# Kernel tuning notes

Measured on AMD Instinct MI355X. Metric: run time of the kernel, lower is better.

## Reference

```python
import jax, jax.numpy as jnp
import numpy as np

NUM_HEADS = 8
NUM_LEVELS = 4
NUM_POINTS = 4
EMBED_DIM = 256
HEAD_DIM = EMBED_DIM // NUM_HEADS  # 32
SUM_POINTS = NUM_LEVELS * NUM_POINTS  # 16
OFFSET_SCALE = 0.5
SPATIAL = [(80, 80), (40, 40), (20, 20), (10, 10)]


def _bilinear_gather(v_flat, x, y, H, W):
    """grid_sample(bilinear, padding zeros, align_corners=False) via gathers.
    v_flat: (BN, c, H*W); x, y: (BN, Lq, P) pixel coords. -> (BN, c, Lq*P)"""
    BN = v_flat.shape[0]
    x0 = jnp.floor(x)
    y0 = jnp.floor(y)
    wx1 = x - x0
    wy1 = y - y0

    def corner(xi, yi, w):
        valid = (xi >= 0) & (xi <= W - 1) & (yi >= 0) & (yi <= H - 1)
        xc = jnp.clip(xi, 0, W - 1).astype(jnp.int32)
        yc = jnp.clip(yi, 0, H - 1).astype(jnp.int32)
        idx = (yc * W + xc).reshape(BN, -1)  # (BN, Lq*P)
        g = jnp.take_along_axis(v_flat, idx[:, None, :], axis=2)  # (BN, c, Lq*P)
        return g * (w * valid).reshape(BN, 1, -1)

    return (corner(x0, y0, (1.0 - wx1) * (1.0 - wy1))
            + corner(x0 + 1.0, y0, wx1 * (1.0 - wy1))
            + corner(x0, y0 + 1.0, (1.0 - wx1) * wy1)
            + corner(x0 + 1.0, y0 + 1.0, wx1 * wy1))


def setup_inputs() -> dict:
    key = jax.random.key(0)
    ks = jax.random.split(key, 6)
    bs, Lq = 16, 300
    spatial = np.array(SPATIAL, dtype=np.int64)
    Lv = int((spatial[:, 0] * spatial[:, 1]).sum())  # 8500

    query = jax.random.normal(ks[0], (bs, Lq, EMBED_DIM), jnp.float32)
    reference_points = jax.random.uniform(ks[1], (bs, Lq, 1, 4), jnp.float32)  # cx,cy,w,h in (0,1)
    value = jax.random.normal(ks[2], (bs, NUM_HEADS, HEAD_DIM, Lv), jnp.float32)

    W_off = jax.random.normal(ks[3], (EMBED_DIM, NUM_HEADS * SUM_POINTS * 2), jnp.float32) * 0.01
    # bias from _reset_parameters grid init
    thetas = np.arange(NUM_HEADS, dtype=np.float32) * (2.0 * np.pi / NUM_HEADS)
    grid = np.stack([np.cos(thetas), np.sin(thetas)], -1)
    grid = grid / np.abs(grid).max(-1, keepdims=True)
    grid = np.tile(grid.reshape(NUM_HEADS, 1, 2), (1, SUM_POINTS, 1))
    scaling = np.concatenate([np.arange(1, NUM_POINTS + 1) for _ in range(NUM_LEVELS)]).reshape(1, -1, 1)
    b_off = jnp.asarray((grid * scaling).reshape(-1), jnp.float32)

    W_attn = jax.random.normal(ks[4], (EMBED_DIM, NUM_HEADS * SUM_POINTS), jnp.float32) * 0.01
    b_attn = jnp.zeros((NUM_HEADS * SUM_POINTS,), jnp.float32)
    num_points_scale = jnp.full((SUM_POINTS,), 1.0 / NUM_POINTS, jnp.float32)

    return {"query": query, "reference_points": reference_points, "value": value,
            "value_spatial_shapes": spatial, "W_off": W_off, "b_off": b_off,
            "W_attn": W_attn, "b_attn": b_attn, "num_points_scale": num_points_scale}


def reference(query, reference_points, value, value_spatial_shapes,
              W_off, b_off, W_attn, b_attn, num_points_scale):
    bs, Lq, _ = query.shape
    BN = bs * NUM_HEADS

    off = (query @ W_off + b_off).reshape(bs, Lq, NUM_HEADS, SUM_POINTS, 2)
    attn = jax.nn.softmax((query @ W_attn + b_attn).reshape(bs, Lq, NUM_HEADS, SUM_POINTS), axis=-1)

    # box branch: reference_points (bs, Lq, 1, 4); [..., 2:] = wh scales offsets
    offset = off * num_points_scale[:, None] * reference_points[:, :, None, :, 2:] * OFFSET_SCALE
    loc = reference_points[:, :, None, :, :2] + offset  # (bs, Lq, H, SUM_POINTS, 2) in [0,1]

    grids = 2.0 * loc - 1.0
    grids = jnp.transpose(grids, (0, 2, 1, 3, 4)).reshape(BN, Lq, SUM_POINTS, 2)
    attn = jnp.transpose(attn, (0, 2, 1, 3)).reshape(BN, 1, Lq, SUM_POINTS)

    shapes = np.asarray(value_spatial_shapes)
    lvl_sizes = (shapes[:, 0] * shapes[:, 1]).tolist()
    v_levels = jnp.split(value.reshape(BN, HEAD_DIM, -1), np.cumsum(lvl_sizes)[:-1], axis=2)
    g_levels = jnp.split(grids, np.arange(NUM_POINTS, SUM_POINTS, NUM_POINTS), axis=2)

    sampled = []
    for (H, W), v_l, g_l in zip(shapes.tolist(), v_levels, g_levels):
        # align_corners=False pixel coords
        x = (g_l[..., 0] + 1.0) * (W * 0.5) - 0.5
        y = (g_l[..., 1] + 1.0) * (H * 0.5) - 0.5
        s = _bilinear_gather(v_l, x, y, H, W).reshape(BN, HEAD_DIM, Lq, NUM_POINTS)
        sampled.append(s)
    sampled = jnp.concatenate(sampled, axis=-1)  # (BN, c, Lq, SUM_POINTS)

    out = (sampled * attn).sum(-1)  # (BN, c, Lq)
    out = out.reshape(bs, NUM_HEADS * HEAD_DIM, Lq).transpose(0, 2, 1)  # (bs, Lq, embed_dim)
    return out
```

## Files before the change

kernel.cpp:

```cpp
#include <hip/hip_runtime.h>
#include <hip/hip_bf16.h>
#include <math.h>

#define BS 16
#define LQ 300
#define NH 8
#define HD 32
#define SP 16
#define ED 256
#define LV 8500
#define NB_BLK 300
#define NTR_BLK (133 * 128)

static __device__ __forceinline__ int imin(int a, int b) { return a < b ? a : b; }
static __device__ __forceinline__ int imax(int a, int b) { return a > b ? a : b; }

static __device__ __forceinline__ unsigned short f2bf(float x) {
    unsigned u = __float_as_uint(x);
    unsigned r = (u + 0x7fffu + ((u >> 16) & 1u)) >> 16;
    return (unsigned short)r;
}

__global__ __launch_bounds__(256) void kF(const float* __restrict__ query,
                                          const float* __restrict__ refp,
                                          const float* __restrict__ Woff,
                                          const float* __restrict__ boff,
                                          const float* __restrict__ Wattn,
                                          const float* __restrict__ battn,
                                          const float* __restrict__ nps,
                                          float* __restrict__ la,
                                          const float* __restrict__ v,
                                          __hip_bfloat16* __restrict__ vt,
                                          int nb) {
    __shared__ float s[16 * 384];
    __shared__ float red[2][16][8][4];
    const int tid = threadIdx.x;

    if ((int)blockIdx.x >= nb) {
        const int t   = blockIdx.x - nb;
        const int bn  = t / 133;
        const int lv0 = (t - bn * 133) * 64;
        float* tile = s;
        {
            const int c  = tid >> 3;
            const int l4 = (tid & 7) * 4;
            const float* src = v + (size_t)bn * (HD * LV) + (size_t)c * LV + lv0;
#pragma unroll
            for (int i = 0; i < 2; ++i) {
                int off = l4 + i * 32;
                if (lv0 + off < LV) {
                    float4 x = *reinterpret_cast<const float4*>(src + off);
                    float* tp = tile + c * 66 + off;
                    *reinterpret_cast<float2*>(tp)     = make_float2(x.x, x.y);
                    *reinterpret_cast<float2*>(tp + 2) = make_float2(x.z, x.w);
                }
            }
        }
        __syncthreads();
        {
            const int lv = tid >> 2;
            const int c8 = (tid & 3) * 8;
            if (lv0 + lv < LV) {
                unsigned pk[4];
#pragma unroll
                for (int j = 0; j < 4; ++j) {
                    float f0 = tile[(c8 + 2 * j) * 66 + lv];
                    float f1 = tile[(c8 + 2 * j + 1) * 66 + lv];
                    pk[j] = (unsigned)f2bf(f0) | ((unsigned)f2bf(f1) << 16);
                }
                uint4 o = make_uint4(pk[0], pk[1], pk[2], pk[3]);
                *reinterpret_cast<uint4*>((char*)vt +
                    ((size_t)bn * LV + lv0 + lv) * (HD * 2) + c8 * 2) = o;
            }
        }
        return;
    }

    float* qbuf = s;
    float* lbuf = s;
    const int gq0 = blockIdx.x * 16;

    const float* qsrc = query + (size_t)gq0 * ED;
#pragma unroll
    for (int i = 0; i < 16; ++i) qbuf[tid + 256 * i] = qsrc[tid + 256 * i];
    __syncthreads();

    const int qi = tid >> 5;
    const int cl = tid & 31;
    const float* qa = qbuf + qi * ED;
    const float* qb = qbuf + (qi + 8) * ED;

    float a0[4] = {0,0,0,0}, a1[4] = {0,0,0,0}, a2[4] = {0,0,0,0};
    float c0[4] = {0,0,0,0}, c1[4] = {0,0,0,0}, c2[4] = {0,0,0,0};
    const float4* w0 = (const float4*)(Woff + cl * 4);
    const float4* w1 = (const float4*)(Woff + 128 + cl * 4);
    const float4* w2 = (const float4*)(Wattn + cl * 4);
#pragma unroll 4
    for (int k = 0; k < ED; ++k) {
        float va = qa[k], vb = qb[k];
        float4 x0 = w0[k * 64];
        float4 x1 = w1[k * 64];
        float4 x2 = w2[k * 32];
        a0[0] += va * x0.x; a0[1] += va * x0.y; a0[2] += va * x0.z; a0[3] += va * x0.w;
        a1[0] += va * x1.x; a1[1] += va * x1.y; a1[2] += va * x1.z; a1[3] += va * x1.w;
        a2[0] += va * x2.x; a2[1] += va * x2.y; a2[2] += va * x2.z; a2[3] += va * x2.w;
        c0[0] += vb * x0.x; c0[1] += vb * x0.y; c0[2] += vb * x0.z; c0[3] += vb * x0.w;
        c1[0] += vb * x1.x; c1[1] += vb * x1.y; c1[2] += vb * x1.z; c1[3] += vb * x1.w;
        c2[0] += vb * x2.x; c2[1] += vb * x2.y; c2[2] += vb * x2.z; c2[3] += vb * x2.w;
    }
    __syncthreads();
    {
        float* ra = lbuf + qi * 384;
        float* rb = lbuf + (qi + 8) * 384;
#pragma unroll
        for (int u = 0; u < 4; ++u) {
            float bo0 = boff[cl * 4 + u];
            float bo1 = boff[128 + cl * 4 + u];
            float ba  = battn[cl * 4 + u];
            ra[cl * 4 + u]       = a0[u] + bo0;
            ra[128 + cl * 4 + u] = a1[u] + bo1;
            ra[256 + cl * 4 + u] = a2[u] + ba;
            rb[cl * 4 + u]       = c0[u] + bo0;
            rb[128 + cl * 4 + u] = c1[u] + bo1;
            rb[256 + cl * 4 + u] = c2[u] + ba;
        }
    }
    __syncthreads();

#pragma unroll
    for (int it = 0; it < 2; ++it) {
        const int slot = it * 256 + tid;
        const int qi2 = slot >> 5;
        const int h2  = (slot >> 2) & 7;
        const int pg  = slot & 3;
        const float* lr = lbuf + qi2 * 384;

        float l[4];
#pragma unroll
        for (int i = 0; i < 4; ++i) l[i] = lr[256 + h2 * 16 + pg * 4 + i];
        float m = fmaxf(fmaxf(l[0], l[1]), fmaxf(l[2], l[3]));
        red[0][qi2][h2][pg] = m;
        __syncthreads();
        m = fmaxf(fmaxf(red[0][qi2][h2][0], red[0][qi2][h2][1]),
                  fmaxf(red[0][qi2][h2][2], red[0][qi2][h2][3]));
        float e[4];
        float ps = 0.f;
#pragma unroll
        for (int i = 0; i < 4; ++i) { e[i] = expf(l[i] - m); ps += e[i]; }
        red[1][qi2][h2][pg] = ps;
        __syncthreads();
        float sden = red[1][qi2][h2][0] + red[1][qi2][h2][1] +
                     red[1][qi2][h2][2] + red[1][qi2][h2][3];
        float inv = 1.f / sden;

        const int gq = gq0 + qi2;
        const int b  = gq / LQ;
        const int q  = gq - b * LQ;
        const float* rp = refp + (size_t)gq * 4;
        float cx = rp[0], cy = rp[1], rw = rp[2], rh = rp[3];

        const int Wl = 80 >> pg;
        const int base = (25600 - (25600 >> (2 * pg))) / 3;
        const float fw = (float)Wl;

        float* dst = la + ((((size_t)b * NH + h2) * LQ + q) * SP + pg * 4) * 8;
#pragma unroll
        for (int i = 0; i < 4; ++i) {
            int p = pg * 4 + i;
            float ox = lr[h2 * 32 + p * 2 + 0];
            float oy = lr[h2 * 32 + p * 2 + 1];
            float sc = nps[p] * 0.5f;
            float locx = cx + ox * sc * rw;
            float locy = cy + oy * sc * rh;
            float x = locx * fw - 0.5f;
            float y = locy * fw - 0.5f;
            float aw = e[i] * inv;

            float x0f = floorf(x), y0f = floorf(y);
            float fx = x - x0f, fy = y - y0f;
            int ix0 = (int)x0f, iy0 = (int)y0f;
            int ix1 = ix0 + 1, iy1 = iy0 + 1;
            bool vx0 = (ix0 >= 0) && (ix0 < Wl);
            bool vx1 = (ix1 >= 0) && (ix1 < Wl);
            bool vy0 = (iy0 >= 0) && (iy0 < Wl);
            bool vy1 = (iy1 >= 0) && (iy1 < Wl);
            int cx0 = imin(imax(ix0, 0), Wl - 1);
            int cx1 = imin(imax(ix1, 0), Wl - 1);
            int cy0 = imin(imax(iy0, 0), Wl - 1);
            int cy1 = imin(imax(iy1, 0), Wl - 1);
            float w00 = aw * (1.f - fx) * (1.f - fy) * ((vx0 && vy0) ? 1.f : 0.f);
            float w10 = aw * fx * (1.f - fy) * ((vx1 && vy0) ? 1.f : 0.f);
            float w01 = aw * (1.f - fx) * fy * ((vx0 && vy1) ? 1.f : 0.f);
            float w11 = aw * fx * fy * ((vx1 && vy1) ? 1.f : 0.f);
            int i00 = base + cy0 * Wl + cx0;
            int i10 = base + cy0 * Wl + cx1;
            int i01 = base + cy1 * Wl + cx0;
            int i11 = base + cy1 * Wl + cx1;

            *reinterpret_cast<float4*>(dst + i * 8) = make_float4(w00, w10, w01, w11);
            *reinterpret_cast<int4*>(dst + i * 8 + 4) = make_int4(i00, i10, i01, i11);
        }
        __syncthreads();
    }
}

__global__ __launch_bounds__(256) void kC3(const __hip_bfloat16* __restrict__ vt,
                                           const float* __restrict__ la,
                                           float* __restrict__ out) {
    __shared__ __align__(16) float sla[64 * 132];
    const int bid = blockIdx.x;
    const int logical = (bid & 7) * 80 + (bid >> 3);
    const int bh = logical / 5;
    const int qt = logical - bh * 5;
    const int b = bh >> 3;
    const int h = bh & 7;
    const int q0 = qt * 64;
    const int nq = imin(64, LQ - q0);

    const int tid = threadIdx.x;
    const float* lsrc = la + ((size_t)bh * LQ + q0) * (SP * 8);
    for (int i = tid; i < nq * 128; i += 256) {
        int r = i >> 7, j = i & 127;
        sla[r * 132 + j] = lsrc[i];
    }
    __syncthreads();

    const int qs = tid >> 2;
    const int l4 = tid & 3;
    if (qs >= nq) return;
    const char* vb = (const char*)vt + (size_t)bh * LV * (HD * 2) + l4 * 16;

    float acc[8] = {0.f, 0.f, 0.f, 0.f, 0.f, 0.f, 0.f, 0.f};
    const float* lq = sla + qs * 132;

#pragma unroll
    for (int p = 0; p < SP; p += 2) {
        float4 wv0 = *reinterpret_cast<const float4*>(lq + p * 8);
        int4  iv0  = *reinterpret_cast<const int4*>(lq + p * 8 + 4);
        float4 wv1 = *reinterpret_cast<const float4*>(lq + p * 8 + 8);
        int4  iv1  = *reinterpret_cast<const int4*>(lq + p * 8 + 12);
        uint4 r0 = *reinterpret_cast<const uint4*>(vb + (size_t)iv0.x * 64);
        uint4 r1 = *reinterpret_cast<const uint4*>(vb + (size_t)iv0.y * 64);
        uint4 r2 = *reinterpret_cast<const uint4*>(vb + (size_t)iv0.z * 64);
        uint4 r3 = *reinterpret_cast<const uint4*>(vb + (size_t)iv0.w * 64);
        uint4 r4 = *reinterpret_cast<const uint4*>(vb + (size_t)iv1.x * 64);
        uint4 r5 = *reinterpret_cast<const uint4*>(vb + (size_t)iv1.y * 64);
        uint4 r6 = *reinterpret_cast<const uint4*>(vb + (size_t)iv1.z * 64);
        uint4 r7 = *reinterpret_cast<const uint4*>(vb + (size_t)iv1.w * 64);
#define FMA8(W, R)                                                             \
        {                                                                      \
            union { unsigned u; float f; } _t;                                 \
            _t.u = (R).x << 16;         acc[0] = fmaf((W), _t.f, acc[0]);      \
            _t.u = (R).x & 0xffff0000u; acc[1] = fmaf((W), _t.f, acc[1]);      \
            _t.u = (R).y << 16;         acc[2] = fmaf((W), _t.f, acc[2]);      \
            _t.u = (R).y & 0xffff0000u; acc[3] = fmaf((W), _t.f, acc[3]);      \
            _t.u = (R).z << 16;         acc[4] = fmaf((W), _t.f, acc[4]);      \
            _t.u = (R).z & 0xffff0000u; acc[5] = fmaf((W), _t.f, acc[5]);      \
            _t.u = (R).w << 16;         acc[6] = fmaf((W), _t.f, acc[6]);      \
            _t.u = (R).w & 0xffff0000u; acc[7] = fmaf((W), _t.f, acc[7]);      \
        }
        FMA8(wv0.x, r0) FMA8(wv0.y, r1) FMA8(wv0.z, r2) FMA8(wv0.w, r3)
        FMA8(wv1.x, r4) FMA8(wv1.y, r5) FMA8(wv1.z, r6) FMA8(wv1.w, r7)
#undef FMA8
    }
    const int q = q0 + qs;
    float* op = out + ((size_t)b * LQ + q) * ED + h * HD + l4 * 8;
    *reinterpret_cast<float4*>(op)     = make_float4(acc[0], acc[1], acc[2], acc[3]);
    *reinterpret_cast<float4*>(op + 4) = make_float4(acc[4], acc[5], acc[6], acc[7]);
}

__global__ __launch_bounds__(320) void kCfb(const float* __restrict__ val,
                                            const float* __restrict__ la,
                                            float* __restrict__ out) {
    __shared__ __align__(16) float sla[10 * SP * 8];
    int bid = blockIdx.x;
    int logical = (bid & 7) * 480 + (bid >> 3);
    int bh = logical / 30;
    int qt = logical - bh * 30;
    int b = bh >> 3;
    int h = bh & 7;
    const int tid = threadIdx.x;
    const float* lsrc = la + (((size_t)bh * LQ + qt * 10) * SP) * 8;
    for (int i = tid; i < 1280; i += 320) sla[i] = lsrc[i];
    __syncthreads();
    const int qs = tid >> 5;
    const int c  = tid & 31;
    const float* vb = val + ((size_t)bh * HD + c) * LV;
    float acc = 0.f;
    const float* lq = sla + qs * (SP * 8);
#pragma unroll
    for (int p = 0; p < SP; ++p) {
        float4 wv = *reinterpret_cast<const float4*>(lq + p * 8);
        int4  iv  = *reinterpret_cast<const int4*>(lq + p * 8 + 4);
        acc += wv.x * vb[iv.x];
        acc += wv.y * vb[iv.y];
        acc += wv.z * vb[iv.z];
        acc += wv.w * vb[iv.w];
    }
    int q = qt * 10 + qs;
    out[((size_t)b * LQ + q) * ED + h * HD + c] = acc;
}

extern "C" void kernel_launch(void* const* d_in, const int* in_sizes, int n_in,
                              void* d_out, int out_size, void* d_ws, size_t ws_size,
                              hipStream_t stream) {
    const float* query = (const float*)d_in[0];
    const float* refp  = (const float*)d_in[1];
    const float* value = (const float*)d_in[2];
    const float* Woff  = (const float*)d_in[4];
    const float* boff  = (const float*)d_in[5];
    const float* Wattn = (const float*)d_in[6];
    const float* battn = (const float*)d_in[7];
    const float* nps   = (const float*)d_in[8];
    float* out = (float*)d_out;

    const size_t la_bytes = (size_t)BS * NH * LQ * SP * 8 * sizeof(float);
    const size_t vt_bytes = (size_t)BS * NH * LV * HD * sizeof(__hip_bfloat16);
    float* la = (float*)d_ws;
    __hip_bfloat16* vt = (__hip_bfloat16*)((char*)d_ws + la_bytes);
    const bool use_tr = ws_size >= la_bytes + vt_bytes;

    if (use_tr) {
        kF<<<dim3(NB_BLK + NTR_BLK), 256, 0, stream>>>(query, refp, Woff, boff,
                                                       Wattn, battn, nps, la,
                                                       value, vt, NB_BLK);
        kC3<<<dim3(640), 256, 0, stream>>>(vt, la, out);
    } else {
        kF<<<dim3(NB_BLK), 256, 0, stream>>>(query, refp, Woff, boff,
                                             Wattn, battn, nps, la,
                                             value, (__hip_bfloat16*)nullptr, NB_BLK);
        kCfb<<<dim3(3840), 320, 0, stream>>>(value, la, out);
    }
}
```

Before: 75.49 us.

## Widen transpose tiles, use shuffle softmax reductions, drop LDS staging in sampler

The value transpose/bf16 conversion blocks now each handle 128 positions instead of 64, halving the transpose block count and issuing all four loads before any LDS stores. The per-head softmax max and sum reductions switch from shared-memory arrays with block barriers to wave shuffles among four adjacent lanes. The sampling kernel drops its shared-memory staging of the location/weight table, reads it directly from global memory with smaller 128-thread blocks and twice as many of them, and partially unrolls the point loop. The intent is less barrier and LDS overhead and higher occupancy, at the cost of uncached global reads of the per-query table.

```diff
diff --git a/kernel.cpp b/kernel.cpp
--- a/kernel.cpp
+++ b/kernel.cpp
@@ -10,7 +10,8 @@
 #define ED 256
 #define LV 8500
 #define NB_BLK 300
-#define NTR_BLK (133 * 128)
+#define TR_PER_BN 67
+#define NTR_BLK (TR_PER_BN * 128)
 
 static __device__ __forceinline__ int imin(int a, int b) { return a < b ? a : b; }
 static __device__ __forceinline__ int imax(int a, int b) { return a > b ? a : b; }
@@ -33,45 +34,46 @@
                                           __hip_bfloat16* __restrict__ vt,
                                           int nb) {
     __shared__ float s[16 * 384];
-    __shared__ float red[2][16][8][4];
     const int tid = threadIdx.x;
 
     if ((int)blockIdx.x >= nb) {
         const int t   = blockIdx.x - nb;
-        const int bn  = t / 133;
-        const int lv0 = (t - bn * 133) * 64;
-        float* tile = s;
-        {
-            const int c  = tid >> 3;
-            const int l4 = (tid & 7) * 4;
-            const float* src = v + (size_t)bn * (HD * LV) + (size_t)c * LV + lv0;
-#pragma unroll
-            for (int i = 0; i < 2; ++i) {
-                int off = l4 + i * 32;
-                if (lv0 + off < LV) {
-                    float4 x = *reinterpret_cast<const float4*>(src + off);
-                    float* tp = tile + c * 66 + off;
-                    *reinterpret_cast<float2*>(tp)     = make_float2(x.x, x.y);
-                    *reinterpret_cast<float2*>(tp + 2) = make_float2(x.z, x.w);
-                }
+        const int bn  = t / TR_PER_BN;
+        const int lv0 = (t - bn * TR_PER_BN) * 128;
+        const int nlv = imin(128, LV - lv0);
+
+        const int c  = tid >> 3;
+        const int l4 = (tid & 7) * 4;
+        const float* src = v + (size_t)bn * (HD * LV) + (size_t)c * LV + lv0;
+        float4 r[4];
+#pragma unroll
+        for (int i = 0; i < 4; ++i) {
+            int off = l4 + 32 * i;
+            if (off < nlv) r[i] = *reinterpret_cast<const float4*>(src + off);
+        }
+        float* tp = s + c * 132;
+#pragma unroll
+        for (int i = 0; i < 4; ++i) {
+            int off = l4 + 32 * i;
+            if (off < nlv) {
+                *reinterpret_cast<float2*>(tp + off)     = make_float2(r[i].x, r[i].y);
+                *reinterpret_cast<float2*>(tp + off + 2) = make_float2(r[i].z, r[i].w);
             }
         }
         __syncthreads();
-        {
-            const int lv = tid >> 2;
-            const int c8 = (tid & 3) * 8;
-            if (lv0 + lv < LV) {
-                unsigned pk[4];
-#pragma unroll
-                for (int j = 0; j < 4; ++j) {
-                    float f0 = tile[(c8 + 2 * j) * 66 + lv];
-                    float f1 = tile[(c8 + 2 * j + 1) * 66 + lv];
-                    pk[j] = (unsigned)f2bf(f0) | ((unsigned)f2bf(f1) << 16);
-                }
-                uint4 o = make_uint4(pk[0], pk[1], pk[2], pk[3]);
-                *reinterpret_cast<uint4*>((char*)vt +
-                    ((size_t)bn * LV + lv0 + lv) * (HD * 2) + c8 * 2) = o;
+        const int lv   = tid >> 1;
+        const int half = (tid & 1) * 16;
+        if (lv < nlv) {
+            unsigned pk[8];
+#pragma unroll
+            for (int j = 0; j < 8; ++j) {
+                float f0 = s[(half + 2 * j) * 132 + lv];
+                float f1 = s[(half + 2 * j + 1) * 132 + lv];
+                pk[j] = (unsigned)f2bf(f0) | ((unsigned)f2bf(f1) << 16);
             }
+            char* dst = (char*)vt + ((size_t)bn * LV + lv0 + lv) * (HD * 2) + half * 2;
+            *reinterpret_cast<uint4*>(dst)      = make_uint4(pk[0], pk[1], pk[2], pk[3]);
+            *reinterpret_cast<uint4*>(dst + 16) = make_uint4(pk[4], pk[5], pk[6], pk[7]);
         }
         return;
     }
@@ -139,19 +141,15 @@
 #pragma unroll
         for (int i = 0; i < 4; ++i) l[i] = lr[256 + h2 * 16 + pg * 4 + i];
         float m = fmaxf(fmaxf(l[0], l[1]), fmaxf(l[2], l[3]));
-        red[0][qi2][h2][pg] = m;
-        __syncthreads();
-        m = fmaxf(fmaxf(red[0][qi2][h2][0], red[0][qi2][h2][1]),
-                  fmaxf(red[0][qi2][h2][2], red[0][qi2][h2][3]));
+        m = fmaxf(m, __shfl_xor(m, 1));
+        m = fmaxf(m, __shfl_xor(m, 2));
         float e[4];
         float ps = 0.f;
 #pragma unroll
         for (int i = 0; i < 4; ++i) { e[i] = expf(l[i] - m); ps += e[i]; }
-        red[1][qi2][h2][pg] = ps;
-        __syncthreads();
-        float sden = red[1][qi2][h2][0] + red[1][qi2][h2][1] +
-                     red[1][qi2][h2][2] + red[1][qi2][h2][3];
-        float inv = 1.f / sden;
+        ps += __shfl_xor(ps, 1);
+        ps += __shfl_xor(ps, 2);
+        float inv = 1.f / ps;
 
         const int gq = gq0 + qi2;
         const int b  = gq / LQ;
@@ -200,40 +198,31 @@
             *reinterpret_cast<float4*>(dst + i * 8) = make_float4(w00, w10, w01, w11);
             *reinterpret_cast<int4*>(dst + i * 8 + 4) = make_int4(i00, i10, i01, i11);
         }
-        __syncthreads();
-    }
-}
-
-__global__ __launch_bounds__(256) void kC3(const __hip_bfloat16* __restrict__ vt,
+    }
+}
+
+__global__ __launch_bounds__(128) void kC4(const __hip_bfloat16* __restrict__ vt,
                                            const float* __restrict__ la,
                                            float* __restrict__ out) {
-    __shared__ __align__(16) float sla[64 * 132];
     const int bid = blockIdx.x;
-    const int logical = (bid & 7) * 80 + (bid >> 3);
-    const int bh = logical / 5;
-    const int qt = logical - bh * 5;
+    const int logical = (bid & 7) * 160 + (bid >> 3);
+    const int bh = logical / 10;
+    const int qt = logical - bh * 10;
     const int b = bh >> 3;
     const int h = bh & 7;
-    const int q0 = qt * 64;
-    const int nq = imin(64, LQ - q0);
 
     const int tid = threadIdx.x;
-    const float* lsrc = la + ((size_t)bh * LQ + q0) * (SP * 8);
-    for (int i = tid; i < nq * 128; i += 256) {
-        int r = i >> 7, j = i & 127;
-        sla[r * 132 + j] = lsrc[i];
-    }
-    __syncthreads();
-
     const int qs = tid >> 2;
     const int l4 = tid & 3;
-    if (qs >= nq) return;
+    const int q = qt * 32 + qs;
+    if (q >= LQ) return;
+
+    const float* lq = la + ((size_t)bh * LQ + q) * (SP * 8);
     const char* vb = (const char*)vt + (size_t)bh * LV * (HD * 2) + l4 * 16;
 
     float acc[8] = {0.f, 0.f, 0.f, 0.f, 0.f, 0.f, 0.f, 0.f};
-    const float* lq = sla + qs * 132;
-
-#pragma unroll
+
+#pragma unroll 2
     for (int p = 0; p < SP; p += 2) {
         float4 wv0 = *reinterpret_cast<const float4*>(lq + p * 8);
         int4  iv0  = *reinterpret_cast<const int4*>(lq + p * 8 + 4);
@@ -263,7 +252,6 @@
         FMA8(wv1.x, r4) FMA8(wv1.y, r5) FMA8(wv1.z, r6) FMA8(wv1.w, r7)
 #undef FMA8
     }
-    const int q = q0 + qs;
     float* op = out + ((size_t)b * LQ + q) * ED + h * HD + l4 * 8;
     *reinterpret_cast<float4*>(op)     = make_float4(acc[0], acc[1], acc[2], acc[3]);
     *reinterpret_cast<float4*>(op + 4) = make_float4(acc[4], acc[5], acc[6], acc[7]);
@@ -324,7 +312,7 @@
         kF<<<dim3(NB_BLK + NTR_BLK), 256, 0, stream>>>(query, refp, Woff, boff,
                                                        Wattn, battn, nps, la,
                                                        value, vt, NB_BLK);
-        kC3<<<dim3(640), 256, 0, stream>>>(vt, la, out);
+        kC4<<<dim3(1280), 128, 0, stream>>>(vt, la, out);
     } else {
         kF<<<dim3(NB_BLK), 256, 0, stream>>>(query, refp, Woff, boff,
                                              Wattn, battn, nps, la,
```

After: 95.62 us. 26.7% more time.
